# Performance work log

Hardware: AMD Instinct MI355X
Metric: run time of the kernel (lower is better)

The kernel has to match this reference:

```python
import jax, jax.numpy as jnp
import numpy as np

HIDDEN = 32
WINDOW = 128
ALPHA = 2.5
T_LEN = 524288


def setup_inputs() -> dict:
    key = jax.random.key(0)
    ks = jax.random.split(key, 9)
    H = HIDDEN
    s = 1.0 / np.sqrt(H)
    u = lambda k, shape: jax.random.uniform(k, shape, jnp.float32, -s, s)
    return {
        "x": jax.random.normal(ks[0], (1, T_LEN, 1), jnp.float32),
        "Wih": u(ks[1], (3 * H, 2)),
        "Whh": u(ks[2], (3 * H, H)),
        "bih": u(ks[3], (3 * H,)),
        "bhh": u(ks[4], (3 * H,)),
        "Wv": u(ks[5], (H, 1)),
        "bv": u(ks[6], (1,)),
        "Ws": u(ks[7], (H, 1)),
        "bs": u(ks[8], (1,)),
    }


def _spike_mask(x1):
    """Vectorized replacement of the per-timestep Python loop.
    mask[t] True iff |x[t] - (2x[t-1]-x[t-2])| > alpha*(sqrt(mean(x[max(0,t-W):t]^2))+1e-8).
    Uses a prefix sum of x^2 for the sliding-window mean. mask[0]=mask[1]=True."""
    T = x1.shape[0]
    cs = jnp.concatenate([jnp.zeros((1,), x1.dtype), jnp.cumsum(x1 * x1)])  # [T+1]
    t = jnp.arange(T)
    ws = jnp.maximum(0, t - WINDOW)
    cnt = jnp.maximum(t - ws, 1).astype(x1.dtype)
    rms = jnp.sqrt(jnp.maximum(cs[t] - cs[ws], 0.0) / cnt) + 1e-8
    pred = 2.0 * jnp.roll(x1, 1) - jnp.roll(x1, 2)  # garbage at t<2, overwritten below
    err = jnp.abs(x1 - pred)
    mask = err > (ALPHA * rms)
    return mask.at[:2].set(True)


def _gru_cell(inp, h, Wih, Whh, bih, bhh):
    H = h.shape[0]
    gi = Wih @ inp + bih  # [3H]
    gh = Whh @ h + bhh    # [3H]
    r = jax.nn.sigmoid(gi[:H] + gh[:H])
    z = jax.nn.sigmoid(gi[H:2 * H] + gh[H:2 * H])
    n = jnp.tanh(gi[2 * H:] + r * gh[2 * H:])
    return (1.0 - z) * n + z * h


def reference(x, Wih, Whh, bih, bhh, Wv, bv, Ws, bs):
    x1 = x[0, :, 0]                       # [T]
    T = x1.shape[0]
    mask = _spike_mask(x1)                # [T] bool (non-differentiable, as in torch detach)
    tf = jnp.arange(T, dtype=x1.dtype)

    # GRU state is only updated at event steps (equivalent to running the GRU over the
    # compacted event sequence); between events the held state is used for linear
    # extrapolation val + slope * (t - t_event)/window.
    def step(carry, inp):
        h, last_t = carry
        xt, m, t = inp
        delta = (t - last_t) / float(WINDOW)
        h_new = _gru_cell(jnp.stack([xt, delta]), h, Wih, Whh, bih, bhh)
        h = jnp.where(m, h_new, h)
        last_t = jnp.where(m, t, last_t)
        dt = (t - last_t) / float(WINDOW)  # 0 at event steps
        out = (h @ Wv + bv) + (h @ Ws + bs) * dt  # [1]
        return (h, last_t), out[0]

    init = (jnp.zeros((HIDDEN,), x1.dtype), jnp.zeros((), x1.dtype))
    _, outs = jax.lax.scan(step, init, (x1, mask, tf))
    output = outs.reshape(1, T, 1)
    N = jnp.sum(mask.astype(jnp.int32))
    return output, N, mask
```

## Files before the change

### kernel.cpp

```cpp
#include <hip/hip_runtime.h>
#include <stdint.h>

#define T_LEN 524288
#define SEG 8
#define WARM 8
#define EPC (SEG + WARM + 1)
#define CHAINS 16
#define GSP (CHAINS * SEG)
#define CBLK 1536

typedef short short8 __attribute__((ext_vector_type(8)));
typedef float f4 __attribute__((ext_vector_type(4)));
#define KEEPA(v) asm volatile("" : "+v"(v))

static const size_t OFF_MASK = 0;
static const size_t OFF_CNT  = T_LEN;
static const size_t OFF_N    = T_LEN + 4096;
static const size_t OFF_SPK  = T_LEN + 8192;

__device__ __forceinline__ short bfr(float f) {
    uint32_t u = __float_as_uint(f);
    u = (u + 0x7fffu + ((u >> 16) & 1u)) >> 16;
    return (short)u;
}

#define IDX(j) ((j) + ((j) >> 5))

__global__ __launch_bounds__(256) void k_mask(const float* __restrict__ x,
                                              uint8_t* __restrict__ mask,
                                              float* __restrict__ out, int out_size,
                                              int* __restrict__ cnt)
{
    __shared__ float tile[1190];
    __shared__ float cs2[1190];
    __shared__ float wsum[4];
    __shared__ int tot;
    const int bs = blockIdx.x * 1024;
    const int tid = threadIdx.x;
    const int lane = tid & 63, w = tid >> 6;
    if (tid == 0) tot = 0;
    for (int j = tid; j < 1154; j += 256) {
        int g = bs - 130 + j;
        tile[IDX(j)] = (g >= 0) ? x[g] : 0.f;
    }
    __syncthreads();

    const int j0 = tid * 5;
    float p[5];
    float run = 0.f;
    #pragma unroll
    for (int k = 0; k < 5; ++k) {
        float v = (j0 + k < 1154) ? tile[IDX(j0 + k)] : 0.f;
        run = fmaf(v, v, run);
        p[k] = run;
    }
    float incl = run;
    for (int d = 1; d < 64; d <<= 1) {
        float u = __shfl_up(incl, d, 64);
        if (lane >= d) incl += u;
    }
    if (lane == 63) wsum[w] = incl;
    __syncthreads();
    float base = incl - run;
    for (int i = 0; i < w; ++i) base += wsum[i];
    #pragma unroll
    for (int k = 0; k < 5; ++k)
        if (j0 + k < 1154) cs2[IDX(j0 + k)] = base + p[k];
    __syncthreads();

    const int loc = tid * 4;
    float tv[6];
    #pragma unroll
    for (int q = 0; q < 6; ++q) tv[q] = tile[IDX(loc + 128 + q)];
    uchar4 mv; float4 mf; int msum = 0;
    uint8_t* mp = &mv.x; float* fp = &mf.x;
    #pragma unroll
    for (int it = 0; it < 4; ++it) {
        int t = bs + loc + it;
        int c = t < 128 ? (t < 1 ? 1 : t) : 128;
        float s = cs2[IDX(loc + 129 + it)] - cs2[IDX(loc + 1 + it)];
        float rms = sqrtf(fmaxf(s, 0.f) / (float)c) + 1e-8f;
        float xt = tv[it + 2];
        float pr = 2.f * tv[it + 1] - tv[it];
        bool m = (t < 2) || (fabsf(xt - pr) > 2.5f * rms);
        mp[it] = m ? 1 : 0; fp[it] = m ? 1.f : 0.f; msum += m ? 1 : 0;
    }
    *(uchar4*)(mask + bs + loc) = mv;
    int oi = T_LEN + 1 + bs + loc;
    if (oi + 3 < out_size) *(float4*)(out + oi) = mf;
    for (int d = 32; d; d >>= 1) msum += __shfl_down(msum, d, 64);
    if ((tid & 63) == 0) atomicAdd(&tot, msum);
    __syncthreads();
    if (tid == 0) cnt[blockIdx.x] = tot;
}

__global__ __launch_bounds__(256) void k_scatter(const uint8_t* __restrict__ mask,
                                                 const int* __restrict__ cnt,
                                                 int* __restrict__ spk,
                                                 int* __restrict__ nspk,
                                                 float* __restrict__ out, int out_size)
{
    __shared__ int wtot[4];
    __shared__ int wpre[4];
    __shared__ int s_base;
    const int tid = threadIdx.x, b = blockIdx.x;

    int pre = 0;
    #pragma unroll
    for (int i = tid; i < 512; i += 256)
        pre += (i < b) ? cnt[i] : 0;
    for (int d = 32; d; d >>= 1) pre += __shfl_down(pre, d, 64);
    if ((tid & 63) == 0) wpre[tid >> 6] = pre;
    __syncthreads();
    if (tid == 0) {
        int t0 = wpre[0] + wpre[1] + wpre[2] + wpre[3];
        s_base = t0;
        if (b == 511) {
            int total = t0 + cnt[511];
            *nspk = total;
            if (T_LEN < out_size) out[T_LEN] = (float)total;
        }
    }

    const int base = b * 1024 + tid * 4;
    uchar4 mv = *(const uchar4*)(mask + base);
    int m0 = mv.x, m1 = mv.y, m2 = mv.z, m3 = mv.w;
    int e1 = m0, e2 = m0 + m1, e3 = m0 + m1 + m2, tsum = e3 + m3;
    int lane = tid & 63, w = tid >> 6;
    int incl = tsum;
    for (int d = 1; d < 64; d <<= 1) {
        int u = __shfl_up(incl, d, 64);
        if (lane >= d) incl += u;
    }
    if (lane == 63) wtot[w] = incl;
    __syncthreads();
    int woff = 0;
    for (int i = 0; i < w; i++) woff += wtot[i];
    int texcl = woff + incl - tsum;
    int g = s_base + texcl;
    int e[4] = {0, e1, e2, e3};
    int m[4] = {m0, m1, m2, m3};
    #pragma unroll
    for (int k = 0; k < 4; k++) {
        if (m[k]) spk[g + e[k]] = base + k;
    }
}

__global__ __attribute__((amdgpu_waves_per_eu(2)))
__launch_bounds__(64)
void k_chain(const float* __restrict__ Whh,
             const float* __restrict__ Wih,
             const float* __restrict__ bih,
             const float* __restrict__ bhh,
             const int* __restrict__ spk,
             const float* __restrict__ x,
             const int* __restrict__ nspk,
             const float* __restrict__ Wv,
             const float* __restrict__ bv,
             const float* __restrict__ Wsc,
             const float* __restrict__ bs,
             float* __restrict__ out)
{
    __shared__ float2   st[CHAINS * EPC];
    __shared__ unsigned hx[CHAINS * 20];
    __shared__ float    ab[2 * GSP];

    const int lane = threadIdx.x;
    const int m = lane & 15;
    const int quad = lane >> 4;
    const int N = *nspk;

    short8 A1[6], A2[6], A3;
    #pragma unroll
    for (int t = 0; t < 6; ++t) {
        union { short s[8]; short8 v; } u1, u2;
        int rowg = 16 * t + m;
        #pragma unroll
        for (int j = 0; j < 8; ++j) {
            int k = 8 * quad + j;
            u1.s[j] = bfr(Whh[rowg * 32 + k]);
            float a2v = 0.f;
            if (k == 0) a2v = Wih[rowg * 2];
            else if (k == 1) a2v = Wih[rowg * 2 + 1];
            else if (k == 2) a2v = (rowg < 64) ? (bih[rowg] + bhh[rowg]) : bih[rowg];
            u2.s[j] = bfr(a2v);
        }
        A1[t] = u1.v; A2[t] = u2.v;
    }
    {
        union { short s[8]; short8 v; } u3;
        #pragma unroll
        for (int j = 0; j < 8; ++j) {
            int k = 8 * quad + j;
            float v = (m == 0) ? Wv[k] : (m == 1) ? Wsc[k] : 0.f;
            u3.s[j] = bfr(v);
        }
        A3 = u3.v;
    }
    #pragma unroll
    for (int t = 0; t < 6; ++t) { KEEPA(A1[t]); KEEPA(A2[t]); }
    KEEPA(A3);

    float bn0[4], bn1[4];
    #pragma unroll
    for (int e = 0; e < 4; ++e) {
        int r0 = quad * 4 + e;
        bn0[e] = bhh[64 + r0];  bn1[e] = bhh[80 + r0];
    }
    const float bv0 = bv[0], bs0 = bs[0];

    for (int g0 = blockIdx.x; g0 * GSP < N; g0 += CBLK) {
        const int base0 = g0 * GSP;
        for (int e = lane; e < CHAINS * EPC; e += 64) {
            int n = e / EPC, j = e - n * EPC;
            int s = base0 + n * SEG - (WARM + 1) + j;
            s = min(max(s, 0), N - 1);
            int t = spk[s];
            st[e] = make_float2((float)t, x[t]);
        }
        __builtin_amdgcn_wave_barrier();

        float h0[4], h1[4];
        #pragma unroll
        for (int e = 0; e < 4; ++e) { h0[e] = 0.f; h1[e] = 0.f; }
        short8 B1 = (short8)0;
        float tprev = st[m * EPC].x;

        for (int j = 0; j < SEG + WARM; ++j) {
            float2 cur = st[m * EPC + j + 1];
            float xt = cur.y;
            float d = (cur.x - tprev) * 0.0078125f;
            tprev = cur.x;

            unsigned p0 = (__float_as_uint(d) & 0xFFFF0000u) | (__float_as_uint(xt) >> 16);
            unsigned p1 = 0x00003F80u;
            p0 = (quad == 0) ? p0 : 0u;
            p1 = (quad == 0) ? p1 : 0u;
            union { unsigned u[4]; short8 v; } b2u;
            b2u.u[0] = p0; b2u.u[1] = p1; b2u.u[2] = 0u; b2u.u[3] = 0u;
            short8 B2 = b2u.v;

            f4 z4 = {0.f, 0.f, 0.f, 0.f};
            f4 Drz[4], Dh0, Dh1, Di0, Di1;
            f4 tmp0 = __builtin_amdgcn_mfma_f32_16x16x32_bf16(A2[0], B2, z4, 0, 0, 0);
            f4 tmp1 = __builtin_amdgcn_mfma_f32_16x16x32_bf16(A2[1], B2, z4, 0, 0, 0);
            f4 tmp2 = __builtin_amdgcn_mfma_f32_16x16x32_bf16(A2[2], B2, z4, 0, 0, 0);
            f4 tmp3 = __builtin_amdgcn_mfma_f32_16x16x32_bf16(A2[3], B2, z4, 0, 0, 0);
            Di0 = __builtin_amdgcn_mfma_f32_16x16x32_bf16(A2[4], B2, z4, 0, 0, 0);
            Di1 = __builtin_amdgcn_mfma_f32_16x16x32_bf16(A2[5], B2, z4, 0, 0, 0);
            Drz[0] = __builtin_amdgcn_mfma_f32_16x16x32_bf16(A1[0], B1, tmp0, 0, 0, 0);
            Drz[1] = __builtin_amdgcn_mfma_f32_16x16x32_bf16(A1[1], B1, tmp1, 0, 0, 0);
            Drz[2] = __builtin_amdgcn_mfma_f32_16x16x32_bf16(A1[2], B1, tmp2, 0, 0, 0);
            Drz[3] = __builtin_amdgcn_mfma_f32_16x16x32_bf16(A1[3], B1, tmp3, 0, 0, 0);
            Dh0 = __builtin_amdgcn_mfma_f32_16x16x32_bf16(A1[4], B1, z4, 0, 0, 0);
            Dh1 = __builtin_amdgcn_mfma_f32_16x16x32_bf16(A1[5], B1, z4, 0, 0, 0);

            #pragma unroll
            for (int e = 0; e < 4; ++e) {
                float r0 = __builtin_amdgcn_rcpf(1.f + __builtin_amdgcn_exp2f(-1.44269504089f * Drz[0][e]));
                float r1 = __builtin_amdgcn_rcpf(1.f + __builtin_amdgcn_exp2f(-1.44269504089f * Drz[1][e]));
                float zz0 = __builtin_amdgcn_rcpf(1.f + __builtin_amdgcn_exp2f(-1.44269504089f * Drz[2][e]));
                float zz1 = __builtin_amdgcn_rcpf(1.f + __builtin_amdgcn_exp2f(-1.44269504089f * Drz[3][e]));
                float np0 = fmaf(r0, Dh0[e] + bn0[e], Di0[e]);
                float np1 = fmaf(r1, Dh1[e] + bn1[e], Di1[e]);
                float en0 = __builtin_amdgcn_exp2f(2.88539008178f * np0);
                float en1 = __builtin_amdgcn_exp2f(2.88539008178f * np1);
                float n0 = fmaf(-2.f, __builtin_amdgcn_rcpf(1.f + en0), 1.f);
                float n1 = fmaf(-2.f, __builtin_amdgcn_rcpf(1.f + en1), 1.f);
                h0[e] = fmaf(zz0, h0[e] - n0, n0);
                h1[e] = fmaf(zz1, h1[e] - n1, n1);
            }

            unsigned q0 = (__float_as_uint(h0[1]) & 0xFFFF0000u) | (__float_as_uint(h0[0]) >> 16);
            unsigned q1 = (__float_as_uint(h0[3]) & 0xFFFF0000u) | (__float_as_uint(h0[2]) >> 16);
            unsigned q2 = (__float_as_uint(h1[1]) & 0xFFFF0000u) | (__float_as_uint(h1[0]) >> 16);
            unsigned q3 = (__float_as_uint(h1[3]) & 0xFFFF0000u) | (__float_as_uint(h1[2]) >> 16);
            *(uint2*)&hx[m * 20 + 2 * quad]     = make_uint2(q0, q1);
            *(uint2*)&hx[m * 20 + 8 + 2 * quad] = make_uint2(q2, q3);
            __builtin_amdgcn_wave_barrier();
            union { uint4 u; short8 v; } bu;
            bu.u = *(const uint4*)&hx[m * 20 + 4 * quad];
            B1 = bu.v;

            if (j >= WARM) {
                f4 Dab = __builtin_amdgcn_mfma_f32_16x16x32_bf16(A3, B1, z4, 0, 0, 0);
                if (quad == 0) {
                    int sg = base0 + m * SEG + (j - WARM);
                    if (sg < N)
                        *(float2*)&ab[2 * (m * SEG + j - WARM)] =
                            make_float2(Dab[0] + bv0, Dab[1] + bs0);
                }
            }
        }
        __builtin_amdgcn_wave_barrier();

        const int nid = base0 + GSP;
        const int tN = (nid >= N) ? T_LEN : spk[nid];
        #pragma unroll
        for (int h = 0; h < 2; ++h) {
            int sl = lane + 64 * h;
            int sg = base0 + sl;
            if (sg < N) {
                int n = sl >> 3, jj = sl & 7;
                float ts = st[n * EPC + (WARM + 1) + jj].x;
                int tnext;
                if (sg + 1 >= N) tnext = T_LEN;
                else if (sl + 1 < GSP) {
                    int n2 = (sl + 1) >> 3, j2 = (sl + 1) & 7;
                    tnext = (int)st[n2 * EPC + (WARM + 1) + j2].x;
                } else tnext = tN;
                float2 abv = *(const float2*)&ab[2 * sl];
                int tsi = (int)ts;
                for (int t = tsi; t < tnext; ++t)
                    out[t] = fmaf(abv.y, (float)(t - tsi) * 0.0078125f, abv.x);
            }
        }
        __builtin_amdgcn_wave_barrier();
    }
}

extern "C" void kernel_launch(void* const* d_in, const int* in_sizes, int n_in,
                              void* d_out, int out_size, void* d_ws, size_t ws_size,
                              hipStream_t stream)
{
    const float* x   = (const float*)d_in[0];
    const float* Wih = (const float*)d_in[1];
    const float* Whh = (const float*)d_in[2];
    const float* bih = (const float*)d_in[3];
    const float* bhh = (const float*)d_in[4];
    const float* Wv  = (const float*)d_in[5];
    const float* bv  = (const float*)d_in[6];
    const float* Wsc = (const float*)d_in[7];
    const float* bs  = (const float*)d_in[8];
    float* out = (float*)d_out;

    char* ws = (char*)d_ws;
    uint8_t* mask = (uint8_t*)(ws + OFF_MASK);
    int* cnt  = (int*)(ws + OFF_CNT);
    int* nspk = (int*)(ws + OFF_N);
    int* spk  = (int*)(ws + OFF_SPK);

    k_mask<<<512, 256, 0, stream>>>(x, mask, out, out_size, cnt);
    k_scatter<<<512, 256, 0, stream>>>(mask, cnt, spk, nspk, out, out_size);
    k_chain<<<CBLK, 64, 0, stream>>>(Whh, Wih, bih, bhh, spk, x, nspk,
                                     Wv, bv, Wsc, bs, out);
}
```

Baseline: 105.2 us.

## Fuse mask, scatter and GRU chain kernels into one cooperative kernel

Merges the three launches (spike mask, prefix-sum scatter, GRU chain evaluation) into a single cooperative kernel that uses grid-wide syncs between phases. The mask bits stay in registers between phases, and GRU weights are loaded into MFMA fragments before the sync. The aim is to remove launch gaps and the mask round-trip through memory. In exchange, the chain phase now runs on 512x4 waves instead of 1536 single-wave blocks, grid.sync adds its own cost, and the old three-kernel path is kept as a fallback if the cooperative launch fails.

```diff
diff --git a/kernel.cpp b/kernel.cpp
--- a/kernel.cpp
+++ b/kernel.cpp
@@ -1,5 +1,8 @@
 #include <hip/hip_runtime.h>
+#include <hip/hip_cooperative_groups.h>
 #include <stdint.h>
+
+namespace cg = cooperative_groups;
 
 #define T_LEN 524288
 #define SEG 8
@@ -7,6 +10,10 @@
 #define EPC (SEG + WARM + 1)
 #define CHAINS 16
 #define GSP (CHAINS * SEG)
+#define NBLK 512
+#define NTHR 256
+#define WPB 4
+#define NWAVE (NBLK * WPB)
 #define CBLK 1536
 
 typedef short short8 __attribute__((ext_vector_type(8)));
@@ -25,6 +32,278 @@
 }
 
 #define IDX(j) ((j) + ((j) >> 5))
+
+struct SMP1 { float tile[1190]; float cs2[1190]; float wsum[4]; };
+struct SMP2 { int wpre[4]; int wall[4]; int wtot[4]; };
+struct SMP3 { float2 st[WPB][CHAINS * EPC]; unsigned hx[WPB][CHAINS * 20]; float ab[WPB][2 * GSP]; };
+union SMU { SMP1 p1; SMP2 p2; SMP3 p3; };
+
+__global__ __launch_bounds__(NTHR, 2)
+void k_fused(const float* __restrict__ x,  const float* __restrict__ Wih,
+             const float* __restrict__ Whh, const float* __restrict__ bih,
+             const float* __restrict__ bhh, const float* __restrict__ Wv,
+             const float* __restrict__ bv,  const float* __restrict__ Wsc,
+             const float* __restrict__ bs,  float* __restrict__ out, int out_size,
+             int* __restrict__ cnt, int* __restrict__ spk)
+{
+    __shared__ SMU sm;
+    __shared__ int s_tot, s_base, s_N;
+    cg::grid_group grid = cg::this_grid();
+
+    const int tid = threadIdx.x;
+    const int lane = tid & 63, w4 = tid >> 6;
+    const int b = blockIdx.x;
+    const int m = lane & 15, quad = lane >> 4;
+
+    if (tid == 0) s_tot = 0;
+    const int mbs = b * 1024;
+    for (int j = tid; j < 1154; j += NTHR) {
+        int g = mbs - 130 + j;
+        sm.p1.tile[IDX(j)] = (g >= 0) ? x[g] : 0.f;
+    }
+    __syncthreads();
+    const int j0 = tid * 5;
+    float p[5]; float run = 0.f;
+    #pragma unroll
+    for (int k = 0; k < 5; ++k) {
+        float v = (j0 + k < 1154) ? sm.p1.tile[IDX(j0 + k)] : 0.f;
+        run = fmaf(v, v, run);
+        p[k] = run;
+    }
+    float incl = run;
+    for (int d = 1; d < 64; d <<= 1) {
+        float u = __shfl_up(incl, d, 64);
+        if (lane >= d) incl += u;
+    }
+    if (lane == 63) sm.p1.wsum[w4] = incl;
+    __syncthreads();
+    float bbase = incl - run;
+    for (int i = 0; i < w4; ++i) bbase += sm.p1.wsum[i];
+    #pragma unroll
+    for (int k = 0; k < 5; ++k)
+        if (j0 + k < 1154) sm.p1.cs2[IDX(j0 + k)] = bbase + p[k];
+    __syncthreads();
+
+    const int loc = tid * 4;
+    float tv[6];
+    #pragma unroll
+    for (int q = 0; q < 6; ++q) tv[q] = sm.p1.tile[IDX(loc + 128 + q)];
+    uchar4 mv; float4 mf; int msum = 0;
+    uint8_t* mp = &mv.x; float* fp = &mf.x;
+    #pragma unroll
+    for (int it = 0; it < 4; ++it) {
+        int t = mbs + loc + it;
+        int c = t < 128 ? (t < 1 ? 1 : t) : 128;
+        float s = sm.p1.cs2[IDX(loc + 129 + it)] - sm.p1.cs2[IDX(loc + 1 + it)];
+        float rms = sqrtf(fmaxf(s, 0.f) / (float)c) + 1e-8f;
+        float xt = tv[it + 2];
+        float pr = 2.f * tv[it + 1] - tv[it];
+        bool mm = (t < 2) || (fabsf(xt - pr) > 2.5f * rms);
+        mp[it] = mm ? 1 : 0; fp[it] = mm ? 1.f : 0.f; msum += mm ? 1 : 0;
+    }
+    int oi = T_LEN + 1 + mbs + loc;
+    if (oi + 3 < out_size) *(float4*)(out + oi) = mf;
+    int msum_r = msum;
+    for (int d = 32; d; d >>= 1) msum_r += __shfl_down(msum_r, d, 64);
+    if (lane == 0) atomicAdd(&s_tot, msum_r);
+    __syncthreads();
+    if (tid == 0) cnt[b] = s_tot;
+
+    short8 A1[6], A2[6], A3;
+    #pragma unroll
+    for (int t = 0; t < 6; ++t) {
+        union { short s[8]; short8 v; } u1, u2;
+        int rowg = 16 * t + m;
+        #pragma unroll
+        for (int j = 0; j < 8; ++j) {
+            int k = 8 * quad + j;
+            u1.s[j] = bfr(Whh[rowg * 32 + k]);
+            float a2v = 0.f;
+            if (k == 0) a2v = Wih[rowg * 2];
+            else if (k == 1) a2v = Wih[rowg * 2 + 1];
+            else if (k == 2) a2v = (rowg < 64) ? (bih[rowg] + bhh[rowg]) : bih[rowg];
+            u2.s[j] = bfr(a2v);
+        }
+        A1[t] = u1.v; A2[t] = u2.v;
+    }
+    {
+        union { short s[8]; short8 v; } u3;
+        #pragma unroll
+        for (int j = 0; j < 8; ++j) {
+            int k = 8 * quad + j;
+            float v = (m == 0) ? Wv[k] : (m == 1) ? Wsc[k] : 0.f;
+            u3.s[j] = bfr(v);
+        }
+        A3 = u3.v;
+    }
+    #pragma unroll
+    for (int t = 0; t < 6; ++t) { KEEPA(A1[t]); KEEPA(A2[t]); }
+    KEEPA(A3);
+    float bn0[4], bn1[4];
+    #pragma unroll
+    for (int e = 0; e < 4; ++e) {
+        int r0 = quad * 4 + e;
+        bn0[e] = bhh[64 + r0];  bn1[e] = bhh[80 + r0];
+    }
+    const float bv0 = bv[0], bs0 = bs[0];
+
+    grid.sync();
+
+    {
+        int v1 = cnt[tid];
+        int v2 = cnt[tid + 256];
+        int pre = ((tid < b) ? v1 : 0) + ((tid + 256 < b) ? v2 : 0);
+        int allv = v1 + v2;
+        for (int d = 32; d; d >>= 1) {
+            pre  += __shfl_down(pre,  d, 64);
+            allv += __shfl_down(allv, d, 64);
+        }
+        if (lane == 0) { sm.p2.wpre[w4] = pre; sm.p2.wall[w4] = allv; }
+        __syncthreads();
+        if (tid == 0) {
+            int sb = sm.p2.wpre[0] + sm.p2.wpre[1] + sm.p2.wpre[2] + sm.p2.wpre[3];
+            int sn = sm.p2.wall[0] + sm.p2.wall[1] + sm.p2.wall[2] + sm.p2.wall[3];
+            s_base = sb; s_N = sn;
+            if (b == NBLK - 1 && T_LEN < out_size) out[T_LEN] = (float)sn;
+        }
+        int m0 = mv.x, m1 = mv.y, m2 = mv.z, m3 = mv.w;
+        int e1 = m0, e2 = m0 + m1, e3 = m0 + m1 + m2, tsum = e3 + m3;
+        int incs = tsum;
+        for (int d = 1; d < 64; d <<= 1) {
+            int u = __shfl_up(incs, d, 64);
+            if (lane >= d) incs += u;
+        }
+        if (lane == 63) sm.p2.wtot[w4] = incs;
+        __syncthreads();
+        int woff = 0;
+        for (int i = 0; i < w4; i++) woff += sm.p2.wtot[i];
+        int texcl = woff + incs - tsum;
+        int g = s_base + texcl;
+        int ee[4] = {0, e1, e2, e3};
+        int mm4[4] = {m0, m1, m2, m3};
+        #pragma unroll
+        for (int k = 0; k < 4; k++) {
+            if (mm4[k]) spk[g + ee[k]] = mbs + loc + k;
+        }
+    }
+
+    grid.sync();
+
+    const int N = s_N;
+    float2*   st = sm.p3.st[w4];
+    unsigned* hx = sm.p3.hx[w4];
+    float*    ab = sm.p3.ab[w4];
+    const int wid = b * WPB + w4;
+
+    for (int g0 = wid; g0 * GSP < N; g0 += NWAVE) {
+        const int base0 = g0 * GSP;
+        for (int e = lane; e < CHAINS * EPC; e += 64) {
+            int n = e / EPC, j = e - n * EPC;
+            int s = base0 + n * SEG - (WARM + 1) + j;
+            s = min(max(s, 0), N - 1);
+            int t = spk[s];
+            st[e] = make_float2((float)t, x[t]);
+        }
+        __builtin_amdgcn_wave_barrier();
+
+        float h0[4], h1[4];
+        #pragma unroll
+        for (int e = 0; e < 4; ++e) { h0[e] = 0.f; h1[e] = 0.f; }
+        short8 B1 = (short8)0;
+        float tprev = st[m * EPC].x;
+
+        for (int j = 0; j < SEG + WARM; ++j) {
+            float2 cur = st[m * EPC + j + 1];
+            float xt = cur.y;
+            float d = (cur.x - tprev) * 0.0078125f;
+            tprev = cur.x;
+
+            unsigned p0 = (__float_as_uint(d) & 0xFFFF0000u) | (__float_as_uint(xt) >> 16);
+            unsigned p1 = 0x00003F80u;
+            p0 = (quad == 0) ? p0 : 0u;
+            p1 = (quad == 0) ? p1 : 0u;
+            union { unsigned u[4]; short8 v; } b2u;
+            b2u.u[0] = p0; b2u.u[1] = p1; b2u.u[2] = 0u; b2u.u[3] = 0u;
+            short8 B2 = b2u.v;
+
+            f4 z4 = {0.f, 0.f, 0.f, 0.f};
+            f4 Drz[4], Dh0, Dh1, Di0, Di1;
+            f4 tmp0 = __builtin_amdgcn_mfma_f32_16x16x32_bf16(A2[0], B2, z4, 0, 0, 0);
+            f4 tmp1 = __builtin_amdgcn_mfma_f32_16x16x32_bf16(A2[1], B2, z4, 0, 0, 0);
+            f4 tmp2 = __builtin_amdgcn_mfma_f32_16x16x32_bf16(A2[2], B2, z4, 0, 0, 0);
+            f4 tmp3 = __builtin_amdgcn_mfma_f32_16x16x32_bf16(A2[3], B2, z4, 0, 0, 0);
+            Di0 = __builtin_amdgcn_mfma_f32_16x16x32_bf16(A2[4], B2, z4, 0, 0, 0);
+            Di1 = __builtin_amdgcn_mfma_f32_16x16x32_bf16(A2[5], B2, z4, 0, 0, 0);
+            Drz[0] = __builtin_amdgcn_mfma_f32_16x16x32_bf16(A1[0], B1, tmp0, 0, 0, 0);
+            Drz[1] = __builtin_amdgcn_mfma_f32_16x16x32_bf16(A1[1], B1, tmp1, 0, 0, 0);
+            Drz[2] = __builtin_amdgcn_mfma_f32_16x16x32_bf16(A1[2], B1, tmp2, 0, 0, 0);
+            Drz[3] = __builtin_amdgcn_mfma_f32_16x16x32_bf16(A1[3], B1, tmp3, 0, 0, 0);
+            Dh0 = __builtin_amdgcn_mfma_f32_16x16x32_bf16(A1[4], B1, z4, 0, 0, 0);
+            Dh1 = __builtin_amdgcn_mfma_f32_16x16x32_bf16(A1[5], B1, z4, 0, 0, 0);
+
+            #pragma unroll
+            for (int e = 0; e < 4; ++e) {
+                float r0 = __builtin_amdgcn_rcpf(1.f + __builtin_amdgcn_exp2f(-1.44269504089f * Drz[0][e]));
+                float r1 = __builtin_amdgcn_rcpf(1.f + __builtin_amdgcn_exp2f(-1.44269504089f * Drz[1][e]));
+                float zz0 = __builtin_amdgcn_rcpf(1.f + __builtin_amdgcn_exp2f(-1.44269504089f * Drz[2][e]));
+                float zz1 = __builtin_amdgcn_rcpf(1.f + __builtin_amdgcn_exp2f(-1.44269504089f * Drz[3][e]));
+                float np0 = fmaf(r0, Dh0[e] + bn0[e], Di0[e]);
+                float np1 = fmaf(r1, Dh1[e] + bn1[e], Di1[e]);
+                float en0 = __builtin_amdgcn_exp2f(2.88539008178f * np0);
+                float en1 = __builtin_amdgcn_exp2f(2.88539008178f * np1);
+                float n0 = fmaf(-2.f, __builtin_amdgcn_rcpf(1.f + en0), 1.f);
+                float n1 = fmaf(-2.f, __builtin_amdgcn_rcpf(1.f + en1), 1.f);
+                h0[e] = fmaf(zz0, h0[e] - n0, n0);
+                h1[e] = fmaf(zz1, h1[e] - n1, n1);
+            }
+
+            unsigned q0 = (__float_as_uint(h0[1]) & 0xFFFF0000u) | (__float_as_uint(h0[0]) >> 16);
+            unsigned q1 = (__float_as_uint(h0[3]) & 0xFFFF0000u) | (__float_as_uint(h0[2]) >> 16);
+            unsigned q2 = (__float_as_uint(h1[1]) & 0xFFFF0000u) | (__float_as_uint(h1[0]) >> 16);
+            unsigned q3 = (__float_as_uint(h1[3]) & 0xFFFF0000u) | (__float_as_uint(h1[2]) >> 16);
+            *(uint2*)&hx[m * 20 + 2 * quad]     = make_uint2(q0, q1);
+            *(uint2*)&hx[m * 20 + 8 + 2 * quad] = make_uint2(q2, q3);
+            __builtin_amdgcn_wave_barrier();
+            union { uint4 u; short8 v; } bu;
+            bu.u = *(const uint4*)&hx[m * 20 + 4 * quad];
+            B1 = bu.v;
+
+            if (j >= WARM) {
+                f4 Dab = __builtin_amdgcn_mfma_f32_16x16x32_bf16(A3, B1, z4, 0, 0, 0);
+                if (quad == 0) {
+                    int sg = base0 + m * SEG + (j - WARM);
+                    if (sg < N)
+                        *(float2*)&ab[2 * (m * SEG + j - WARM)] =
+                            make_float2(Dab[0] + bv0, Dab[1] + bs0);
+                }
+            }
+        }
+        __builtin_amdgcn_wave_barrier();
+
+        const int nid = base0 + GSP;
+        const int tN = (nid >= N) ? T_LEN : spk[nid];
+        #pragma unroll
+        for (int h = 0; h < 2; ++h) {
+            int sl = lane + 64 * h;
+            int sg = base0 + sl;
+            if (sg < N) {
+                int n = sl >> 3, jj = sl & 7;
+                float ts = st[n * EPC + (WARM + 1) + jj].x;
+                int tnext;
+                if (sg + 1 >= N) tnext = T_LEN;
+                else if (sl + 1 < GSP) {
+                    int n2 = (sl + 1) >> 3, j2 = (sl + 1) & 7;
+                    tnext = (int)st[n2 * EPC + (WARM + 1) + j2].x;
+                } else tnext = tN;
+                float2 abv = *(const float2*)&ab[2 * sl];
+                int tsi = (int)ts;
+                for (int t = tsi; t < tnext; ++t)
+                    out[t] = fmaf(abv.y, (float)(t - tsi) * 0.0078125f, abv.x);
+            }
+        }
+        __builtin_amdgcn_wave_barrier();
+    }
+}
 
 __global__ __launch_bounds__(256) void k_mask(const float* __restrict__ x,
                                               uint8_t* __restrict__ mask,
@@ -44,7 +323,6 @@
         tile[IDX(j)] = (g >= 0) ? x[g] : 0.f;
     }
     __syncthreads();
-
     const int j0 = tid * 5;
     float p[5];
     float run = 0.f;
@@ -104,7 +382,6 @@
     __shared__ int wpre[4];
     __shared__ int s_base;
     const int tid = threadIdx.x, b = blockIdx.x;
-
     int pre = 0;
     #pragma unroll
     for (int i = tid; i < 512; i += 256)
@@ -121,7 +398,6 @@
             if (T_LEN < out_size) out[T_LEN] = (float)total;
         }
     }
-
     const int base = b * 1024 + tid * 4;
     uchar4 mv = *(const uchar4*)(mask + base);
     int m0 = mv.x, m1 = mv.y, m2 = mv.z, m3 = mv.w;
@@ -340,8 +616,20 @@
     int* nspk = (int*)(ws + OFF_N);
     int* spk  = (int*)(ws + OFF_SPK);
 
-    k_mask<<<512, 256, 0, stream>>>(x, mask, out, out_size, cnt);
-    k_scatter<<<512, 256, 0, stream>>>(mask, cnt, spk, nspk, out, out_size);
-    k_chain<<<CBLK, 64, 0, stream>>>(Whh, Wih, bih, bhh, spk, x, nspk,
-                                     Wv, bv, Wsc, bs, out);
+    void* ka[13];
+    ka[0]  = (void*)&x;   ka[1]  = (void*)&Wih; ka[2]  = (void*)&Whh;
+    ka[3]  = (void*)&bih; ka[4]  = (void*)&bhh; ka[5]  = (void*)&Wv;
+    ka[6]  = (void*)&bv;  ka[7]  = (void*)&Wsc; ka[8]  = (void*)&bs;
+    ka[9]  = (void*)&out; ka[10] = (void*)&out_size;
+    ka[11] = (void*)&cnt; ka[12] = (void*)&spk;
+
+    hipError_t err = hipLaunchCooperativeKernel((const void*)k_fused,
+                                                dim3(NBLK), dim3(NTHR),
+                                                ka, 0, stream);
+    if (err != hipSuccess) {
+        k_mask<<<512, 256, 0, stream>>>(x, mask, out, out_size, cnt);
+        k_scatter<<<512, 256, 0, stream>>>(mask, cnt, spk, nspk, out, out_size);
+        k_chain<<<CBLK, 64, 0, stream>>>(Whh, Wih, bih, bhh, spk, x, nspk,
+                                         Wv, bv, Wsc, bs, out);
+    }
 }
```

After: 231.1 us. 120% more time.

## Fuse spike scatter into chain kernel by compacting mask chunks on the fly

Applied to the files above, without the earlier changes.

Removes the separate scatter kernel that built a compacted spike-index array. Each chain block now computes a prefix sum of per-chunk counts itself, finds the mask chunks covering its event range, and compacts the events directly into shared memory with popcount and wave scans. This saves one launch and the global spike-index round trip. In exchange, every block redoes the 512-entry prefix scan and rescans whole 1024-element mask chunks, which may be redundant when events are sparse.

```diff
diff --git a/kernel.cpp b/kernel.cpp
--- a/kernel.cpp
+++ b/kernel.cpp
@@ -8,6 +8,7 @@
 #define CHAINS 16
 #define GSP (CHAINS * SEG)
 #define CBLK 1536
+#define NCH 512
 
 typedef short short8 __attribute__((ext_vector_type(8)));
 typedef float f4 __attribute__((ext_vector_type(4)));
@@ -15,8 +16,6 @@
 
 static const size_t OFF_MASK = 0;
 static const size_t OFF_CNT  = T_LEN;
-static const size_t OFF_N    = T_LEN + 4096;
-static const size_t OFF_SPK  = T_LEN + 8192;
 
 __device__ __forceinline__ short bfr(float f) {
     uint32_t u = __float_as_uint(f);
@@ -94,81 +93,46 @@
     if (tid == 0) cnt[blockIdx.x] = tot;
 }
 
-__global__ __launch_bounds__(256) void k_scatter(const uint8_t* __restrict__ mask,
-                                                 const int* __restrict__ cnt,
-                                                 int* __restrict__ spk,
-                                                 int* __restrict__ nspk,
-                                                 float* __restrict__ out, int out_size)
-{
-    __shared__ int wtot[4];
-    __shared__ int wpre[4];
-    __shared__ int s_base;
-    const int tid = threadIdx.x, b = blockIdx.x;
-
-    int pre = 0;
-    #pragma unroll
-    for (int i = tid; i < 512; i += 256)
-        pre += (i < b) ? cnt[i] : 0;
-    for (int d = 32; d; d >>= 1) pre += __shfl_down(pre, d, 64);
-    if ((tid & 63) == 0) wpre[tid >> 6] = pre;
-    __syncthreads();
-    if (tid == 0) {
-        int t0 = wpre[0] + wpre[1] + wpre[2] + wpre[3];
-        s_base = t0;
-        if (b == 511) {
-            int total = t0 + cnt[511];
-            *nspk = total;
-            if (T_LEN < out_size) out[T_LEN] = (float)total;
-        }
-    }
-
-    const int base = b * 1024 + tid * 4;
-    uchar4 mv = *(const uchar4*)(mask + base);
-    int m0 = mv.x, m1 = mv.y, m2 = mv.z, m3 = mv.w;
-    int e1 = m0, e2 = m0 + m1, e3 = m0 + m1 + m2, tsum = e3 + m3;
-    int lane = tid & 63, w = tid >> 6;
-    int incl = tsum;
-    for (int d = 1; d < 64; d <<= 1) {
-        int u = __shfl_up(incl, d, 64);
-        if (lane >= d) incl += u;
-    }
-    if (lane == 63) wtot[w] = incl;
-    __syncthreads();
-    int woff = 0;
-    for (int i = 0; i < w; i++) woff += wtot[i];
-    int texcl = woff + incl - tsum;
-    int g = s_base + texcl;
-    int e[4] = {0, e1, e2, e3};
-    int m[4] = {m0, m1, m2, m3};
-    #pragma unroll
-    for (int k = 0; k < 4; k++) {
-        if (m[k]) spk[g + e[k]] = base + k;
-    }
-}
-
 __global__ __attribute__((amdgpu_waves_per_eu(2)))
 __launch_bounds__(64)
 void k_chain(const float* __restrict__ Whh,
              const float* __restrict__ Wih,
              const float* __restrict__ bih,
              const float* __restrict__ bhh,
-             const int* __restrict__ spk,
+             const uint8_t* __restrict__ mask,
+             const int* __restrict__ cnt,
              const float* __restrict__ x,
-             const int* __restrict__ nspk,
              const float* __restrict__ Wv,
              const float* __restrict__ bv,
              const float* __restrict__ Wsc,
              const float* __restrict__ bs,
-             float* __restrict__ out)
+             float* __restrict__ out, int out_size)
 {
     __shared__ float2   st[CHAINS * EPC];
     __shared__ unsigned hx[CHAINS * 20];
     __shared__ float    ab[2 * GSP];
+    __shared__ int      P[NCH + 1];
+    __shared__ int      tn_sh;
 
     const int lane = threadIdx.x;
     const int m = lane & 15;
     const int quad = lane >> 4;
-    const int N = *nspk;
+
+    int vv[8]; int locs = 0;
+    #pragma unroll
+    for (int k = 0; k < 8; ++k) { vv[k] = cnt[lane * 8 + k]; locs += vv[k]; }
+    int incp = locs;
+    for (int d = 1; d < 64; d <<= 1) {
+        int u = __shfl_up(incp, d, 64);
+        if (lane >= d) incp += u;
+    }
+    int runp = incp - locs;
+    #pragma unroll
+    for (int k = 0; k < 8; ++k) { P[lane * 8 + k] = runp; runp += vv[k]; }
+    if (lane == 63) P[NCH] = incp;
+    __builtin_amdgcn_wave_barrier();
+    const int N = P[NCH];
+    if (blockIdx.x == 0 && lane == 0 && T_LEN < out_size) out[T_LEN] = (float)N;
 
     short8 A1[6], A2[6], A3;
     #pragma unroll
@@ -211,14 +175,75 @@
 
     for (int g0 = blockIdx.x; g0 * GSP < N; g0 += CBLK) {
         const int base0 = g0 * GSP;
-        for (int e = lane; e < CHAINS * EPC; e += 64) {
-            int n = e / EPC, j = e - n * EPC;
-            int s = base0 + n * SEG - (WARM + 1) + j;
-            s = min(max(s, 0), N - 1);
-            int t = spk[s];
-            st[e] = make_float2((float)t, x[t]);
+        const int s_lo = base0 - (WARM + 1);
+        const int s_hi = base0 + GSP;
+        const int s_lo_c = max(s_lo, 0);
+        const int s_hi_c = min(s_hi, N - 1);
+
+        if (lane == 0) tn_sh = T_LEN;
+        if (s_lo < 0) {
+            float x0 = x[0];
+            for (int e = lane; e < CHAINS * EPC; e += 64) {
+                int n = e / EPC, j = e - n * EPC;
+                int s = base0 + n * SEG - (WARM + 1) + j;
+                if (s < 0) st[e] = make_float2(0.f, x0);
+            }
+        }
+
+        int c0 = -1, c1 = -1;
+        #pragma unroll
+        for (int k = 0; k < 8; ++k) {
+            int c = lane * 8 + k;
+            if (P[c] <= s_lo_c && s_lo_c < P[c + 1]) c0 = c;
+            if (P[c] <= s_hi_c && s_hi_c < P[c + 1]) c1 = c;
+        }
+        for (int d = 32; d; d >>= 1) {
+            c0 = max(c0, __shfl_down(c0, d, 64));
+            c1 = max(c1, __shfl_down(c1, d, 64));
+        }
+        c0 = __shfl(c0, 0, 64);
+        c1 = __shfl(c1, 0, 64);
+
+        for (int c = c0; c <= c1; ++c) {
+            const uint8_t* mp = mask + c * 1024 + lane * 16;
+            uint4 mw = *(const uint4*)mp;
+            int cl = __popc(mw.x) + __popc(mw.y) + __popc(mw.z) + __popc(mw.w);
+            int ic = cl;
+            for (int d = 1; d < 64; d <<= 1) {
+                int u = __shfl_up(ic, d, 64);
+                if (lane >= d) ic += u;
+            }
+            int s = P[c] + ic - cl;
+            unsigned wds[4] = {mw.x, mw.y, mw.z, mw.w};
+            #pragma unroll
+            for (int wq = 0; wq < 4; ++wq) {
+                unsigned W = wds[wq];
+                #pragma unroll
+                for (int by = 0; by < 4; ++by) {
+                    if ((W >> (8 * by)) & 1u) {
+                        if (s >= s_lo_c && s <= s_hi_c) {
+                            int t = c * 1024 + lane * 16 + wq * 4 + by;
+                            int rel = s - base0;
+                            if (rel == GSP) {
+                                tn_sh = t;
+                            } else {
+                                float xv = x[t];
+                                int n_lo = rel >> 3;
+                                int n_hi = (rel + 9) >> 3;
+                                n_lo = max(n_lo, 0); n_hi = min(n_hi, CHAINS - 1);
+                                for (int n = n_lo; n <= n_hi; ++n) {
+                                    int j = rel + (WARM + 1) - SEG * n;
+                                    st[n * EPC + j] = make_float2((float)t, xv);
+                                }
+                            }
+                        }
+                        ++s;
+                    }
+                }
+            }
         }
         __builtin_amdgcn_wave_barrier();
+        const int tN = tn_sh;
 
         float h0[4], h1[4];
         #pragma unroll
@@ -294,8 +319,6 @@
         }
         __builtin_amdgcn_wave_barrier();
 
-        const int nid = base0 + GSP;
-        const int tN = (nid >= N) ? T_LEN : spk[nid];
         #pragma unroll
         for (int h = 0; h < 2; ++h) {
             int sl = lane + 64 * h;
@@ -337,11 +360,8 @@
     char* ws = (char*)d_ws;
     uint8_t* mask = (uint8_t*)(ws + OFF_MASK);
     int* cnt  = (int*)(ws + OFF_CNT);
-    int* nspk = (int*)(ws + OFF_N);
-    int* spk  = (int*)(ws + OFF_SPK);
 
     k_mask<<<512, 256, 0, stream>>>(x, mask, out, out_size, cnt);
-    k_scatter<<<512, 256, 0, stream>>>(mask, cnt, spk, nspk, out, out_size);
-    k_chain<<<CBLK, 64, 0, stream>>>(Whh, Wih, bih, bhh, spk, x, nspk,
-                                     Wv, bv, Wsc, bs, out);
+    k_chain<<<CBLK, 64, 0, stream>>>(Whh, Wih, bih, bhh, mask, cnt, x,
+                                     Wv, bv, Wsc, bs, out, out_size);
 }
```

After: 108.8 us. +3.4%, slower.
